# Optimization experiments

Hardware: AMD Instinct MI355X
Metric: run time of the kernel (lower is better)

The kernel has to match this reference:

```python
import jax, jax.numpy as jnp
import numpy as np

B, P, D = 16, 512, 1024   # batch, num wordpieces, bert_dim (roberta-large)
W, T, E = 400, 32, 64     # num words, num triggers (spans), num entities (spans)
H = 600                   # hidden_num of role_idn_ffn


def _make_idxs(rng, b, m, n, max_len):
    # [start, end) intervals with 0 <= start < end <= n, sorted starts per row
    starts = np.sort(rng.integers(0, n - 1, size=(b, m)), axis=1)
    ends = np.minimum(starts + rng.integers(1, max_len + 1, size=(b, m)), n)
    ends = np.maximum(ends, starts + 1)
    return np.stack([starts, ends], axis=-1).astype(np.int32)


def setup_inputs() -> dict:
    key = jax.random.key(0)
    k1, k2, k3 = jax.random.split(key, 3)
    rng = np.random.default_rng(0)
    return {
        "piece_reprs": jax.random.normal(k1, (B, P, D), dtype=jnp.float32),
        "word_idxs": jnp.asarray(_make_idxs(rng, B, W, P, 4)),
        "trigger_idxs": jnp.asarray(_make_idxs(rng, B, T, W, 8)),
        "entity_idxs": jnp.asarray(_make_idxs(rng, B, E, W, 12)),
        "W0": jax.random.normal(k2, (4 * D, H), dtype=jnp.float32) * 0.02,
        "b0": jnp.zeros((H,), dtype=jnp.float32),
        "W1": jax.random.normal(k3, (H, 2), dtype=jnp.float32) * 0.02,
        "b1": jnp.zeros((2,), dtype=jnp.float32),
    }


def _segment_mean(x, idxs):
    """Mean of x[b, start:end] per interval. x: [B,N,Dm], idxs: [B,M,2] -> [B,M,Dm].
    Vectorized replacement of the nested-loop slice+mean via inclusive prefix sums."""
    cs = jnp.concatenate([jnp.zeros_like(x[:, :1]), jnp.cumsum(x, axis=1)], axis=1)  # [B,N+1,Dm]
    s = jnp.take_along_axis(cs, idxs[:, :, 0:1], axis=1)  # [B,M,Dm]
    e = jnp.take_along_axis(cs, idxs[:, :, 1:2], axis=1)  # [B,M,Dm]
    lens = (idxs[:, :, 1] - idxs[:, :, 0]).astype(x.dtype)[:, :, None]
    return (e - s) / lens


def reference(piece_reprs, word_idxs, trigger_idxs, entity_idxs, W0, b0, W1, b1):
    # encode(): wordpiece -> word averaging (compute_word_reps_avg)
    word_reprs = _segment_mean(piece_reprs, word_idxs)          # [B, W, D]
    # scores(): span mean pooling (compute_span_reprs)
    trig = _segment_mean(word_reprs, trigger_idxs)              # [B, T, D]
    ent = _segment_mean(word_reprs, entity_idxs)                # [B, E, D]
    b, t, d = trig.shape
    e = ent.shape[1]
    # compute_binary_reprs: all (trigger, entity) pairs, trigger index varies slowly
    t_rep = jnp.broadcast_to(trig[:, :, None, :], (b, t, e, d)).reshape(b, t * e, d)
    e_rep = jnp.broadcast_to(ent[:, None, :, :], (b, t, e, d)).reshape(b, t * e, d)
    role = jnp.concatenate([t_rep, e_rep, t_rep * e_rep, jnp.abs(t_rep - e_rep)], axis=-1)  # [B,T*E,4D]
    # role_idn_ffn: Linears([4D, H, 2]) with relu between layers (dropout=0 at eval)
    h = jax.nn.relu(role @ W0 + b0)
    return h @ W1 + b1                                          # [B, T*E, 2]
```

## Files before the change

### kernel.cpp

```cpp
#include <hip/hip_runtime.h>
#include <cstddef>
#include <cstdint>

typedef float f32x4 __attribute__((ext_vector_type(4)));
typedef __bf16 bf16x8 __attribute__((ext_vector_type(8)));

constexpr int NB = 16;
constexpr int NP = 512;
constexpr int ND = 1024;
constexpr int NW = 400;
constexpr int NT = 32;
constexpr int NE = 64;
constexpr int NH = 600;
constexpr int IMGP = 128 * 64;
constexpr int IMGQ = 320 * 32;

__device__ inline bf16x8 pack8(float a0, float a1, float a2, float a3,
                               float a4, float a5, float a6, float a7) {
    bf16x8 v;
    v[0] = (__bf16)a0; v[1] = (__bf16)a1; v[2] = (__bf16)a2; v[3] = (__bf16)a3;
    v[4] = (__bf16)a4; v[5] = (__bf16)a5; v[6] = (__bf16)a6; v[7] = (__bf16)a7;
    return v;
}

__device__ inline void dma16(const void* g, void* l) {
    __builtin_amdgcn_global_load_lds(
        (const __attribute__((address_space(1))) uint32_t*)g,
        (__attribute__((address_space(3))) uint32_t*)l, 16, 0, 0);
}

#define LGKM_BARRIER() \
    asm volatile("s_waitcnt lgkmcnt(0)\n\ts_barrier" ::: "memory")

template <int MAXW>
__device__ inline float4 span_mean_cols(const float* __restrict__ pbase,
                                        const int* __restrict__ wrow,
                                        int s, int e) {
    int nw = e - s;
    int ps[MAXW], pe[MAXW];
#pragma unroll
    for (int w = 0; w < MAXW; ++w) {
        bool act = w < nw;
        int ww = s + w;
        ps[w] = act ? wrow[2 * ww] : 0;
        pe[w] = act ? wrow[2 * ww + 1] : 0;
    }
    float4 acc = make_float4(0.f, 0.f, 0.f, 0.f);
#pragma unroll
    for (int cb = 0; cb < MAXW; cb += 4) {
#pragma unroll
        for (int w = cb; w < cb + 4; ++w) {
            float4 wa = make_float4(0.f, 0.f, 0.f, 0.f);
#pragma unroll
            for (int p = 0; p < 4; ++p) {
                if (ps[w] + p < pe[w]) {
                    float4 v =
                        *(const float4*)(pbase + (size_t)(ps[w] + p) * ND);
                    wa.x += v.x; wa.y += v.y; wa.z += v.z; wa.w += v.w;
                }
            }
            if (pe[w] > ps[w]) {
                float wi = 1.0f / (float)(pe[w] - ps[w]);
                acc.x += wa.x * wi; acc.y += wa.y * wi;
                acc.z += wa.z * wi; acc.w += wa.w * wi;
            }
        }
    }
    return acc;
}

__global__ __launch_bounds__(256) void prep_kernel(
    const float* __restrict__ piece, const int* __restrict__ widx,
    const int* __restrict__ tidx, const int* __restrict__ eidx,
    const float* __restrict__ W0, __bf16* __restrict__ W0pre,
    __bf16* __restrict__ W0pair, float* __restrict__ trig,
    float* __restrict__ ent, float* __restrict__ out, int out_size) {
    __shared__ float T[32][132];
    int id = blockIdx.x;
    int t = threadIdx.x;
    if (id < NB * (NT + NE)) {
        const int* idx;
        float* outp;
        int b;
        bool is_trig = id < NB * NT;
        if (is_trig) {
            b = id / NT; idx = tidx + id * 2; outp = trig + (size_t)id * ND;
        } else {
            int id2 = id - NB * NT;
            b = id2 / NE; idx = eidx + id2 * 2; outp = ent + (size_t)id2 * ND;
        }
        int s = idx[0], e = idx[1];
        int col = t * 4;
        const int* wrow = widx + b * NW * 2;
        const float* pbase = piece + (size_t)b * NP * ND + col;
        float4 acc = is_trig ? span_mean_cols<8>(pbase, wrow, s, e)
                             : span_mean_cols<12>(pbase, wrow, s, e);
        float inv = 1.0f / (float)(e - s);
        acc.x *= inv; acc.y *= inv; acc.z *= inv; acc.w *= inv;
        *(float4*)(outp + col) = acc;
    } else {
        int bid = id - NB * (NT + NE);
        if (bid < 160) {
            int kb = bid & 31, nc = bid >> 5;
            __bf16* img = W0pre + ((size_t)nc * 32 + kb) * IMGP;
#pragma unroll
            for (int h = 0; h < 2; ++h) {
                {
                    int kl = t >> 3;
                    int n0 = (t & 7) * 16;
                    int kg = kb * 64 + h * 32 + kl;
                    const float* src = W0 + (size_t)kg * NH + nc * 128 + n0;
#pragma unroll
                    for (int g = 0; g < 4; ++g) {
                        int n = nc * 128 + n0 + g * 4;
                        float4 v = (n < NH) ? *(const float4*)(src + g * 4)
                                            : make_float4(0.f, 0.f, 0.f, 0.f);
                        *(float4*)&T[kl][n0 + g * 4] = v;
                    }
                }
                __syncthreads();
#pragma unroll
                for (int s = 0; s < 2; ++s) {
                    int idx = s * 256 + t;
                    int row = idx >> 2, cl = idx & 3, c = h * 4 + cl;
                    bf16x8 v = pack8(T[cl * 8 + 0][row], T[cl * 8 + 1][row],
                                     T[cl * 8 + 2][row], T[cl * 8 + 3][row],
                                     T[cl * 8 + 4][row], T[cl * 8 + 5][row],
                                     T[cl * 8 + 6][row], T[cl * 8 + 7][row]);
                    *(bf16x8*)&img[row * 64 + ((c ^ (row & 7)) << 3)] = v;
                }
                __syncthreads();
            }
        } else if (bid < 672) {
            int e = bid - 160;
            int it = e & 63, nc = (e >> 6) & 1, zz = e >> 7;
            float (*Tp)[84] = reinterpret_cast<float(*)[84]>(&T[0][0]);
            {
                int kidx = t >> 3, part = t & 7;
                int korig = (kidx < 16) ? (2048 + it * 16 + kidx)
                                        : (3072 + it * 16 + (kidx - 16));
                const float* src = W0 + (size_t)korig * NH;
#pragma unroll
                for (int g = 0; g < 10; ++g) {
                    int n = nc * 320 + zz * 80 + part * 10 + g;
                    Tp[kidx][part * 10 + g] = (n < NH) ? src[n] : 0.0f;
                }
            }
            __syncthreads();
            __bf16* img = W0pair + ((size_t)nc * 64 + it) * IMGQ;
#pragma unroll
            for (int s = 0; s < 2; ++s) {
                int idx = s * 256 + t;
                if (idx < 320) {
                    int rloc = idx >> 2, c = idx & 3;
                    bf16x8 v = pack8(Tp[c * 8 + 0][rloc], Tp[c * 8 + 1][rloc],
                                     Tp[c * 8 + 2][rloc], Tp[c * 8 + 3][rloc],
                                     Tp[c * 8 + 4][rloc], Tp[c * 8 + 5][rloc],
                                     Tp[c * 8 + 6][rloc], Tp[c * 8 + 7][rloc]);
                    int rg = zz * 80 + rloc;
                    int slot = ((rg >> 1) + c) & 3;
                    *(bf16x8*)&img[rg * 32 + slot * 8] = v;
                }
            }
        } else {
            int j = ((bid - 672) * 256 + t) * 8;
            float4 z = make_float4(0.f, 0.f, 0.f, 0.f);
            if (j + 8 <= out_size) {
                *(float4*)(out + j) = z;
                *(float4*)(out + j + 4) = z;
            }
        }
    }
}

__global__ __launch_bounds__(256) void pre_mfma_kernel(
    const float* __restrict__ trig, const float* __restrict__ ent,
    const __bf16* __restrict__ W0pre, float* __restrict__ pre_t,
    float* __restrict__ pre_e) {
    __shared__ __bf16 As[2][64 * 64];
    __shared__ __bf16 Bs[3][64 * 64];
    int mt8 = blockIdx.x, ntile = blockIdx.y;
    const float* A;
    float* C;
    int kbofs, mbase;
    if (mt8 < 8) { A = trig; C = pre_t; kbofs = 0;  mbase = mt8 * 64; }
    else         { A = ent;  C = pre_e; kbofs = 16; mbase = (mt8 - 8) * 64; }
    int tid = threadIdx.x;
    int lane = tid & 63, w = tid >> 6, rw = w & 1, cw = w >> 1;
    int q = lane >> 4, l15 = lane & 15, sa = l15 & 7;
    int nc = ntile >> 1, half = ntile & 1;
    const __bf16* imgbase =
        W0pre + ((size_t)nc * 32 + kbofs) * IMGP + half * 4096;
    int ar = tid >> 2, seg = tid & 3;
    f32x4 acc[2][2] = {};
    float4 av[4];

    auto dma_bb = [&](int it, int buf) {
        const __bf16* img = imgbase + (size_t)it * IMGP;
#pragma unroll
        for (int i = 0; i < 2; ++i) {
            int idx = i * 4 + w;
            dma16(img + idx * 512 + lane * 8, (__bf16*)Bs[buf] + idx * 512);
        }
    };
    auto load_a = [&](int it) {
        const float* src = A + (size_t)(mbase + ar) * ND + it * 64;
#pragma unroll
        for (int i = 0; i < 2; ++i) {
            int c = seg * 2 + i;
            av[i * 2]     = *(const float4*)(src + c * 8);
            av[i * 2 + 1] = *(const float4*)(src + c * 8 + 4);
        }
    };
    auto write_a = [&](int buf) {
#pragma unroll
        for (int i = 0; i < 2; ++i) {
            int c = seg * 2 + i;
            float4 a0 = av[i * 2], a1 = av[i * 2 + 1];
            *(bf16x8*)&As[buf][ar * 64 + ((c ^ (ar & 7)) << 3)] =
                pack8(a0.x, a0.y, a0.z, a0.w, a1.x, a1.y, a1.z, a1.w);
        }
    };
    auto mfma_t = [&](int abuf, int bbuf) {
#pragma unroll
        for (int ks = 0; ks < 2; ++ks) {
            int coff = ((q ^ sa) ^ (ks << 2)) << 3;
            bf16x8 af[2];
#pragma unroll
            for (int mt = 0; mt < 2; ++mt)
                af[mt] = *(const bf16x8*)&As[abuf][(32 * rw + 16 * mt + l15) * 64 + coff];
#pragma unroll
            for (int nt = 0; nt < 2; ++nt) {
                bf16x8 bf = *(const bf16x8*)&Bs[bbuf][(32 * cw + 16 * nt + l15) * 64 + coff];
#pragma unroll
                for (int mt = 0; mt < 2; ++mt)
                    acc[mt][nt] = __builtin_amdgcn_mfma_f32_16x16x32_bf16(
                        af[mt], bf, acc[mt][nt], 0, 0, 0);
            }
        }
    };

    load_a(0);
    dma_bb(0, 0);
    dma_bb(1, 1);
    write_a(0);
    __syncthreads();

    int bc = 0, bp = 2;
    for (int it = 0; it < 16; ++it) {
        int acur = it & 1, anxt = acur ^ 1;
        if (it < 15) load_a(it + 1);
        if (it < 14) dma_bb(it + 2, bp);
        __builtin_amdgcn_s_setprio(1);
        mfma_t(acur, bc);
        __builtin_amdgcn_s_setprio(0);
        if (it < 15) write_a(anxt);
        LGKM_BARRIER();
        bc = (bc == 2) ? 0 : bc + 1;
        bp = (bp == 2) ? 0 : bp + 1;
    }

#pragma unroll
    for (int mt = 0; mt < 2; ++mt)
#pragma unroll
        for (int r = 0; r < 4; ++r) {
            float* crow =
                C + (size_t)(mbase + 32 * rw + 16 * mt + 4 * q + r) * NH;
#pragma unroll
            for (int nt = 0; nt < 2; ++nt) {
                int n = ntile * 64 + 32 * cw + 16 * nt + l15;
                if (n < NH) crow[n] = acc[mt][nt][r];
            }
        }
}

__global__ __launch_bounds__(256, 2) void pair_mfma_kernel(
    const float* __restrict__ trig, const float* __restrict__ ent,
    const __bf16* __restrict__ W0pair, const float* __restrict__ b0,
    const float* __restrict__ pre_t, const float* __restrict__ pre_e,
    const float* __restrict__ W1, const float* __restrict__ b1,
    float* __restrict__ out) {
    __shared__ __bf16 Xs[2][128 * 32];
    __shared__ __bf16 Bs[2][320 * 32];
    __shared__ float Ts[2048];
    int b = blockIdx.x, tp = blockIdx.y, nc = blockIdx.z;
    int tid = threadIdx.x;
    int lane = tid & 63, w = tid >> 6, rw = w & 1, cw = w >> 1;
    int q = lane >> 4, l15 = lane & 15;
    int xr = tid >> 1, xh = tid & 1;
    const float* t0row = trig + (size_t)(b * NT + tp * 2) * ND;
    const float* erow = ent + (size_t)(b * NE + (xr & 63)) * ND;
    const __bf16* imgbase = W0pair + (size_t)nc * 64 * IMGQ;
    f32x4 acc[4][10] = {};
    float4 efA0, efA1, efB0, efB1;

    auto dma_b = [&](int it, int buf) {
        const __bf16* img = imgbase + (size_t)it * IMGQ + w * 2560;
        __bf16* lds = &Bs[buf][w * 2560];
#pragma unroll
        for (int i = 0; i < 5; ++i)
            dma16(img + i * 512 + lane * 8, lds + i * 512);
    };
    auto load_eA = [&](int it) {
        const float* er = erow + it * 16 + xh * 8;
        efA0 = *(const float4*)er;
        efA1 = *(const float4*)(er + 4);
    };
    auto load_eB = [&](int it) {
        const float* er = erow + it * 16 + xh * 8;
        efB0 = *(const float4*)er;
        efB1 = *(const float4*)(er + 4);
    };
    auto write_x = [&](int it, int buf, float4 e0, float4 e1) {
        const float* tsp = &Ts[(xr >> 6) * 1024 + it * 16 + xh * 8];
        float4 t0 = *(const float4*)tsp;
        float4 t1 = *(const float4*)(tsp + 4);
        float tf[8], ef[8];
        tf[0] = t0.x; tf[1] = t0.y; tf[2] = t0.z; tf[3] = t0.w;
        tf[4] = t1.x; tf[5] = t1.y; tf[6] = t1.z; tf[7] = t1.w;
        ef[0] = e0.x; ef[1] = e0.y; ef[2] = e0.z; ef[3] = e0.w;
        ef[4] = e1.x; ef[5] = e1.y; ef[6] = e1.z; ef[7] = e1.w;
        int sp = (((xr >> 1) + xh) & 3) * 8;
        int sd = (((xr >> 1) + 2 + xh) & 3) * 8;
        __bf16* xb = &Xs[buf][xr * 32];
        *(bf16x8*)(xb + sp) = pack8(
            tf[0] * ef[0], tf[1] * ef[1], tf[2] * ef[2], tf[3] * ef[3],
            tf[4] * ef[4], tf[5] * ef[5], tf[6] * ef[6], tf[7] * ef[7]);
        *(bf16x8*)(xb + sd) = pack8(
            fabsf(tf[0] - ef[0]), fabsf(tf[1] - ef[1]),
            fabsf(tf[2] - ef[2]), fabsf(tf[3] - ef[3]),
            fabsf(tf[4] - ef[4]), fabsf(tf[5] - ef[5]),
            fabsf(tf[6] - ef[6]), fabsf(tf[7] - ef[7]));
    };
    auto mfma_tile = [&](int buf) {
        const __bf16* X = Xs[buf];
        const __bf16* Bb = Bs[buf];
        bf16x8 af[4];
#pragma unroll
        for (int mt = 0; mt < 4; ++mt) {
            int r = 64 * rw + 16 * mt + l15;
            af[mt] = *(const bf16x8*)&X[r * 32 + (((r >> 1) + q) & 3) * 8];
        }
        __builtin_amdgcn_s_setprio(1);
#pragma unroll
        for (int nt = 0; nt < 10; ++nt) {
            int r = 160 * cw + 16 * nt + l15;
            bf16x8 bv = *(const bf16x8*)&Bb[r * 32 + (((r >> 1) + q) & 3) * 8];
#pragma unroll
            for (int mt = 0; mt < 4; ++mt)
                acc[mt][nt] = __builtin_amdgcn_mfma_f32_16x16x32_bf16(
                    af[mt], bv, acc[mt][nt], 0, 0, 0);
        }
        __builtin_amdgcn_s_setprio(0);
    };

    {
        int k0 = (tid & 127) * 8;
        int row = tid >> 7;
        const float* src = t0row + row * ND + k0;
        float4 va = *(const float4*)src;
        float4 vb = *(const float4*)(src + 4);
        *(float4*)&Ts[row * 1024 + k0] = va;
        *(float4*)&Ts[row * 1024 + k0 + 4] = vb;
    }
    load_eA(0);
    dma_b(0, 0);
    __syncthreads();
    load_eB(1);
    write_x(0, 0, efA0, efA1);
    __syncthreads();

    for (int itp = 0; itp < 32; ++itp) {
        int it0 = itp * 2;
        int it1 = it0 + 1;
        if (it0 < 62) load_eA(it0 + 2);
        dma_b(it0 + 1, 1);
        write_x(it0 + 1, 1, efB0, efB1);
        mfma_tile(0);
        __syncthreads();
        if (it1 < 62) load_eB(it1 + 2);
        if (it1 < 63) {
            dma_b(it1 + 1, 0);
            write_x(it1 + 1, 0, efA0, efA1);
        }
        mfma_tile(1);
        __syncthreads();
    }

    int tglob = b * NT + tp * 2 + rw;
    const float* preT = pre_t + (size_t)tglob * NH;
    float w10[10], w11[10], b0v[10], ptv[10];
    int nbase = nc * 320 + 160 * cw + l15;
#pragma unroll
    for (int nt = 0; nt < 10; ++nt) {
        int n = nbase + 16 * nt;
        bool v = n < NH;
        w10[nt] = v ? W1[2 * n] : 0.f;
        w11[nt] = v ? W1[2 * n + 1] : 0.f;
        b0v[nt] = v ? b0[n] : 0.f;
        ptv[nt] = v ? preT[n] : 0.f;
    }
    float b10 = b1[0], b11 = b1[1];
    bool lead = (l15 == 0);
    bool addb = (nc == 0) && (cw == 0);
#pragma unroll
    for (int mt = 0; mt < 4; ++mt) {
#pragma unroll
        for (int r = 0; r < 4; ++r) {
            int e = 16 * mt + 4 * q + r;
            const float* preE = pre_e + (size_t)(b * NE + e) * NH;
            float s0 = 0.f, s1 = 0.f;
#pragma unroll
            for (int nt = 0; nt < 10; ++nt) {
                int n = nbase + 16 * nt;
                float pe = (n < NH) ? preE[n] : 0.f;
                float h = acc[mt][nt][r] + ptv[nt] + pe + b0v[nt];
                h = fmaxf(h, 0.f);
                s0 += h * w10[nt];
                s1 += h * w11[nt];
            }
#pragma unroll
            for (int m = 8; m >= 1; m >>= 1) {
                s0 += __shfl_xor(s0, m);
                s1 += __shfl_xor(s1, m);
            }
            if (lead) {
                if (addb) { s0 += b10; s1 += b11; }
                float* o = out + ((size_t)(tglob * NE + e)) * 2;
                atomicAdd(o, s0);
                atomicAdd(o + 1, s1);
            }
        }
    }
}

extern "C" void kernel_launch(void* const* d_in, const int* in_sizes, int n_in,
                              void* d_out, int out_size, void* d_ws,
                              size_t ws_size, hipStream_t stream) {
    const float* piece = (const float*)d_in[0];
    const int* widx = (const int*)d_in[1];
    const int* tidx = (const int*)d_in[2];
    const int* eidx = (const int*)d_in[3];
    const float* W0 = (const float*)d_in[4];
    const float* b0 = (const float*)d_in[5];
    const float* W1 = (const float*)d_in[6];
    const float* b1 = (const float*)d_in[7];
    float* out = (float*)d_out;

    float* ws = (float*)d_ws;
    float* trig = ws;
    float* ent = trig + (size_t)NB * NT * ND;
    float* pre_t = ent + (size_t)NB * NE * ND;
    float* pre_e = pre_t + (size_t)NB * NT * NH;
    __bf16* W0pre = (__bf16*)(pre_e + (size_t)NB * NE * NH);
    __bf16* W0pair = W0pre + (size_t)5 * 32 * IMGP;

    int nprep = NB * (NT + NE) + 704;
    prep_kernel<<<nprep, 256, 0, stream>>>(piece, widx, tidx, eidx, W0, W0pre,
                                           W0pair, trig, ent, out, out_size);
    pre_mfma_kernel<<<dim3(24, 10), 256, 0, stream>>>(trig, ent, W0pre,
                                                      pre_t, pre_e);
    pair_mfma_kernel<<<dim3(16, 16, 2), 256, 0, stream>>>(
        trig, ent, W0pair, b0, pre_t, pre_e, W1, b1, out);
}
```

Before: 203.9 us.

## Split pair MFMA blocks to one trigger each for higher occupancy

Each pair_mfma block now handles a single trigger (64 pair rows) instead of two, doubling the grid to 16x32x2. The per-wave accumulator tile shrinks from 4x10 to 4x5 MFMA tiles and LDS usage drops, so launch bounds rise to 3 blocks per CU. The cost is that the W0pair B tiles are streamed twice as often, since each block reuses them across half as many rows, and there are more atomics per output element.

```diff
diff --git a/kernel.cpp b/kernel.cpp
--- a/kernel.cpp
+++ b/kernel.cpp
@@ -274,24 +274,25 @@
         }
 }
 
-__global__ __launch_bounds__(256, 2) void pair_mfma_kernel(
+__global__ __launch_bounds__(256, 3) void pair_mfma_kernel(
     const float* __restrict__ trig, const float* __restrict__ ent,
     const __bf16* __restrict__ W0pair, const float* __restrict__ b0,
     const float* __restrict__ pre_t, const float* __restrict__ pre_e,
     const float* __restrict__ W1, const float* __restrict__ b1,
     float* __restrict__ out) {
-    __shared__ __bf16 Xs[2][128 * 32];
+    __shared__ __bf16 Xs[2][64 * 32];
     __shared__ __bf16 Bs[2][320 * 32];
-    __shared__ float Ts[2048];
+    __shared__ float Ts[1024];
     int b = blockIdx.x, tp = blockIdx.y, nc = blockIdx.z;
     int tid = threadIdx.x;
-    int lane = tid & 63, w = tid >> 6, rw = w & 1, cw = w >> 1;
+    int lane = tid & 63, w = tid >> 6;
+    int cw = w;
     int q = lane >> 4, l15 = lane & 15;
-    int xr = tid >> 1, xh = tid & 1;
-    const float* t0row = trig + (size_t)(b * NT + tp * 2) * ND;
-    const float* erow = ent + (size_t)(b * NE + (xr & 63)) * ND;
+    int xr = tid >> 2, xq = tid & 3;
+    const float* t0row = trig + (size_t)(b * NT + tp) * ND;
+    const float* erow = ent + (size_t)(b * NE + xr) * ND;
     const __bf16* imgbase = W0pair + (size_t)nc * 64 * IMGQ;
-    f32x4 acc[4][10] = {};
+    f32x4 acc[4][5] = {};
     float4 efA0, efA1, efB0, efB1;
 
     auto dma_b = [&](int it, int buf) {
@@ -302,17 +303,17 @@
             dma16(img + i * 512 + lane * 8, lds + i * 512);
     };
     auto load_eA = [&](int it) {
-        const float* er = erow + it * 16 + xh * 8;
+        const float* er = erow + it * 16 + (xq & 1) * 8;
         efA0 = *(const float4*)er;
         efA1 = *(const float4*)(er + 4);
     };
     auto load_eB = [&](int it) {
-        const float* er = erow + it * 16 + xh * 8;
+        const float* er = erow + it * 16 + (xq & 1) * 8;
         efB0 = *(const float4*)er;
         efB1 = *(const float4*)(er + 4);
     };
     auto write_x = [&](int it, int buf, float4 e0, float4 e1) {
-        const float* tsp = &Ts[(xr >> 6) * 1024 + it * 16 + xh * 8];
+        const float* tsp = &Ts[it * 16 + (xq & 1) * 8];
         float4 t0 = *(const float4*)tsp;
         float4 t1 = *(const float4*)(tsp + 4);
         float tf[8], ef[8];
@@ -320,17 +321,17 @@
         tf[4] = t1.x; tf[5] = t1.y; tf[6] = t1.z; tf[7] = t1.w;
         ef[0] = e0.x; ef[1] = e0.y; ef[2] = e0.z; ef[3] = e0.w;
         ef[4] = e1.x; ef[5] = e1.y; ef[6] = e1.z; ef[7] = e1.w;
-        int sp = (((xr >> 1) + xh) & 3) * 8;
-        int sd = (((xr >> 1) + 2 + xh) & 3) * 8;
-        __bf16* xb = &Xs[buf][xr * 32];
-        *(bf16x8*)(xb + sp) = pack8(
-            tf[0] * ef[0], tf[1] * ef[1], tf[2] * ef[2], tf[3] * ef[3],
-            tf[4] * ef[4], tf[5] * ef[5], tf[6] * ef[6], tf[7] * ef[7]);
-        *(bf16x8*)(xb + sd) = pack8(
-            fabsf(tf[0] - ef[0]), fabsf(tf[1] - ef[1]),
-            fabsf(tf[2] - ef[2]), fabsf(tf[3] - ef[3]),
-            fabsf(tf[4] - ef[4]), fabsf(tf[5] - ef[5]),
-            fabsf(tf[6] - ef[6]), fabsf(tf[7] - ef[7]));
+        bool prod = (xq < 2);
+        float vj[8];
+#pragma unroll
+        for (int j = 0; j < 8; ++j) {
+            float p = tf[j] * ef[j];
+            float d = fabsf(tf[j] - ef[j]);
+            vj[j] = prod ? p : d;
+        }
+        int slot = ((xr >> 1) + xq) & 3;
+        *(bf16x8*)&Xs[buf][xr * 32 + slot * 8] =
+            pack8(vj[0], vj[1], vj[2], vj[3], vj[4], vj[5], vj[6], vj[7]);
     };
     auto mfma_tile = [&](int buf) {
         const __bf16* X = Xs[buf];
@@ -338,13 +339,13 @@
         bf16x8 af[4];
 #pragma unroll
         for (int mt = 0; mt < 4; ++mt) {
-            int r = 64 * rw + 16 * mt + l15;
+            int r = 16 * mt + l15;
             af[mt] = *(const bf16x8*)&X[r * 32 + (((r >> 1) + q) & 3) * 8];
         }
         __builtin_amdgcn_s_setprio(1);
 #pragma unroll
-        for (int nt = 0; nt < 10; ++nt) {
-            int r = 160 * cw + 16 * nt + l15;
+        for (int nt = 0; nt < 5; ++nt) {
+            int r = 80 * cw + 16 * nt + l15;
             bf16x8 bv = *(const bf16x8*)&Bb[r * 32 + (((r >> 1) + q) & 3) * 8];
 #pragma unroll
             for (int mt = 0; mt < 4; ++mt)
@@ -354,15 +355,7 @@
         __builtin_amdgcn_s_setprio(0);
     };
 
-    {
-        int k0 = (tid & 127) * 8;
-        int row = tid >> 7;
-        const float* src = t0row + row * ND + k0;
-        float4 va = *(const float4*)src;
-        float4 vb = *(const float4*)(src + 4);
-        *(float4*)&Ts[row * 1024 + k0] = va;
-        *(float4*)&Ts[row * 1024 + k0 + 4] = vb;
-    }
+    *(float4*)&Ts[tid * 4] = *(const float4*)(t0row + tid * 4);
     load_eA(0);
     dma_b(0, 0);
     __syncthreads();
@@ -387,12 +380,12 @@
         __syncthreads();
     }
 
-    int tglob = b * NT + tp * 2 + rw;
+    int tglob = b * NT + tp;
     const float* preT = pre_t + (size_t)tglob * NH;
-    float w10[10], w11[10], b0v[10], ptv[10];
-    int nbase = nc * 320 + 160 * cw + l15;
-#pragma unroll
-    for (int nt = 0; nt < 10; ++nt) {
+    float w10[5], w11[5], b0v[5], ptv[5];
+    int nbase = nc * 320 + 80 * cw + l15;
+#pragma unroll
+    for (int nt = 0; nt < 5; ++nt) {
         int n = nbase + 16 * nt;
         bool v = n < NH;
         w10[nt] = v ? W1[2 * n] : 0.f;
@@ -411,7 +404,7 @@
             const float* preE = pre_e + (size_t)(b * NE + e) * NH;
             float s0 = 0.f, s1 = 0.f;
 #pragma unroll
-            for (int nt = 0; nt < 10; ++nt) {
+            for (int nt = 0; nt < 5; ++nt) {
                 int n = nbase + 16 * nt;
                 float pe = (n < NH) ? preE[n] : 0.f;
                 float h = acc[mt][nt][r] + ptv[nt] + pe + b0v[nt];
@@ -460,6 +453,6 @@
                                            W0pair, trig, ent, out, out_size);
     pre_mfma_kernel<<<dim3(24, 10), 256, 0, stream>>>(trig, ent, W0pre,
                                                       pre_t, pre_e);
-    pair_mfma_kernel<<<dim3(16, 16, 2), 256, 0, stream>>>(
+    pair_mfma_kernel<<<dim3(16, 32, 2), 256, 0, stream>>>(
         trig, ent, W0pair, b0, pre_t, pre_e, W1, b1, out);
 }
```

New measurement: 245.2 us. +20.3%, slower.

## Build MFMA A-fragments in registers instead of staging pair features in LDS

Applied to the files above, without the earlier changes.

The product and abs-difference pair features are now computed straight into each lane's MFMA A operand: every lane loads its own entity rows from global memory and the trigger slice from LDS. This removes the Xs shared buffer, its writes and reads, and one barrier per k-step, and simplifies the loop to one iteration per k-step. In exchange each lane issues more global loads (four entity rows per step, redundant across waves), holds more registers, and computes both product and difference only to select one. Entity loads are now prefetched just one step ahead, so less latency is hidden.

```diff
diff --git a/kernel.cpp b/kernel.cpp
--- a/kernel.cpp
+++ b/kernel.cpp
@@ -280,19 +280,22 @@
     const float* __restrict__ pre_t, const float* __restrict__ pre_e,
     const float* __restrict__ W1, const float* __restrict__ b1,
     float* __restrict__ out) {
-    __shared__ __bf16 Xs[2][128 * 32];
     __shared__ __bf16 Bs[2][320 * 32];
     __shared__ float Ts[2048];
     int b = blockIdx.x, tp = blockIdx.y, nc = blockIdx.z;
     int tid = threadIdx.x;
     int lane = tid & 63, w = tid >> 6, rw = w & 1, cw = w >> 1;
     int q = lane >> 4, l15 = lane & 15;
-    int xr = tid >> 1, xh = tid & 1;
+    int kh = q & 1;
+    bool prod = (q < 2);
     const float* t0row = trig + (size_t)(b * NT + tp * 2) * ND;
-    const float* erow = ent + (size_t)(b * NE + (xr & 63)) * ND;
     const __bf16* imgbase = W0pair + (size_t)nc * 64 * IMGQ;
+    const float* ep0 = ent + (size_t)(b * NE + 0 + l15) * ND + kh * 8;
+    const float* ep1 = ep0 + 16 * ND;
+    const float* ep2 = ep0 + 32 * ND;
+    const float* ep3 = ep0 + 48 * ND;
     f32x4 acc[4][10] = {};
-    float4 efA0, efA1, efB0, efB1;
+    float4 ea0, ea1, eb0, eb1, ec0, ec1, ed0, ed1;
 
     auto dma_b = [&](int it, int buf) {
         const __bf16* img = imgbase + (size_t)it * IMGQ + w * 2560;
@@ -301,57 +304,28 @@
         for (int i = 0; i < 5; ++i)
             dma16(img + i * 512 + lane * 8, lds + i * 512);
     };
-    auto load_eA = [&](int it) {
-        const float* er = erow + it * 16 + xh * 8;
-        efA0 = *(const float4*)er;
-        efA1 = *(const float4*)(er + 4);
-    };
-    auto load_eB = [&](int it) {
-        const float* er = erow + it * 16 + xh * 8;
-        efB0 = *(const float4*)er;
-        efB1 = *(const float4*)(er + 4);
-    };
-    auto write_x = [&](int it, int buf, float4 e0, float4 e1) {
-        const float* tsp = &Ts[(xr >> 6) * 1024 + it * 16 + xh * 8];
-        float4 t0 = *(const float4*)tsp;
-        float4 t1 = *(const float4*)(tsp + 4);
-        float tf[8], ef[8];
-        tf[0] = t0.x; tf[1] = t0.y; tf[2] = t0.z; tf[3] = t0.w;
-        tf[4] = t1.x; tf[5] = t1.y; tf[6] = t1.z; tf[7] = t1.w;
-        ef[0] = e0.x; ef[1] = e0.y; ef[2] = e0.z; ef[3] = e0.w;
-        ef[4] = e1.x; ef[5] = e1.y; ef[6] = e1.z; ef[7] = e1.w;
-        int sp = (((xr >> 1) + xh) & 3) * 8;
-        int sd = (((xr >> 1) + 2 + xh) & 3) * 8;
-        __bf16* xb = &Xs[buf][xr * 32];
-        *(bf16x8*)(xb + sp) = pack8(
-            tf[0] * ef[0], tf[1] * ef[1], tf[2] * ef[2], tf[3] * ef[3],
-            tf[4] * ef[4], tf[5] * ef[5], tf[6] * ef[6], tf[7] * ef[7]);
-        *(bf16x8*)(xb + sd) = pack8(
-            fabsf(tf[0] - ef[0]), fabsf(tf[1] - ef[1]),
-            fabsf(tf[2] - ef[2]), fabsf(tf[3] - ef[3]),
-            fabsf(tf[4] - ef[4]), fabsf(tf[5] - ef[5]),
-            fabsf(tf[6] - ef[6]), fabsf(tf[7] - ef[7]));
-    };
-    auto mfma_tile = [&](int buf) {
-        const __bf16* X = Xs[buf];
-        const __bf16* Bb = Bs[buf];
-        bf16x8 af[4];
-#pragma unroll
-        for (int mt = 0; mt < 4; ++mt) {
-            int r = 64 * rw + 16 * mt + l15;
-            af[mt] = *(const bf16x8*)&X[r * 32 + (((r >> 1) + q) & 3) * 8];
-        }
-        __builtin_amdgcn_s_setprio(1);
-#pragma unroll
-        for (int nt = 0; nt < 10; ++nt) {
-            int r = 160 * cw + 16 * nt + l15;
-            bf16x8 bv = *(const bf16x8*)&Bb[r * 32 + (((r >> 1) + q) & 3) * 8];
-#pragma unroll
-            for (int mt = 0; mt < 4; ++mt)
-                acc[mt][nt] = __builtin_amdgcn_mfma_f32_16x16x32_bf16(
-                    af[mt], bv, acc[mt][nt], 0, 0, 0);
-        }
-        __builtin_amdgcn_s_setprio(0);
+    auto load_e = [&](int it) {
+        const float* p0 = ep0 + it * 16;
+        ea0 = *(const float4*)p0;  ea1 = *(const float4*)(p0 + 4);
+        const float* p1 = ep1 + it * 16;
+        eb0 = *(const float4*)p1;  eb1 = *(const float4*)(p1 + 4);
+        const float* p2 = ep2 + it * 16;
+        ec0 = *(const float4*)p2;  ec1 = *(const float4*)(p2 + 4);
+        const float* p3 = ep3 + it * 16;
+        ed0 = *(const float4*)p3;  ed1 = *(const float4*)(p3 + 4);
+    };
+    auto mk_af = [&](const float* tf, float4 x0, float4 x1) -> bf16x8 {
+        float e[8];
+        e[0] = x0.x; e[1] = x0.y; e[2] = x0.z; e[3] = x0.w;
+        e[4] = x1.x; e[5] = x1.y; e[6] = x1.z; e[7] = x1.w;
+        float v[8];
+#pragma unroll
+        for (int j = 0; j < 8; ++j) {
+            float p = tf[j] * e[j];
+            float d = fabsf(tf[j] - e[j]);
+            v[j] = prod ? p : d;
+        }
+        return pack8(v[0], v[1], v[2], v[3], v[4], v[5], v[6], v[7]);
     };
 
     {
@@ -363,27 +337,42 @@
         *(float4*)&Ts[row * 1024 + k0] = va;
         *(float4*)&Ts[row * 1024 + k0 + 4] = vb;
     }
-    load_eA(0);
+    load_e(0);
     dma_b(0, 0);
     __syncthreads();
-    load_eB(1);
-    write_x(0, 0, efA0, efA1);
-    __syncthreads();
-
-    for (int itp = 0; itp < 32; ++itp) {
-        int it0 = itp * 2;
-        int it1 = it0 + 1;
-        if (it0 < 62) load_eA(it0 + 2);
-        dma_b(it0 + 1, 1);
-        write_x(it0 + 1, 1, efB0, efB1);
-        mfma_tile(0);
-        __syncthreads();
-        if (it1 < 62) load_eB(it1 + 2);
-        if (it1 < 63) {
-            dma_b(it1 + 1, 0);
-            write_x(it1 + 1, 0, efA0, efA1);
-        }
-        mfma_tile(1);
+
+    for (int it = 0; it < 64; ++it) {
+        int cur = it & 1;
+        if (it < 63) dma_b(it + 1, cur ^ 1);
+        bf16x8 af[4];
+        {
+            const float* tsp = &Ts[rw * 1024 + it * 16 + kh * 8];
+            float4 t0 = *(const float4*)tsp;
+            float4 t1 = *(const float4*)(tsp + 4);
+            float tf[8];
+            tf[0] = t0.x; tf[1] = t0.y; tf[2] = t0.z; tf[3] = t0.w;
+            tf[4] = t1.x; tf[5] = t1.y; tf[6] = t1.z; tf[7] = t1.w;
+            af[0] = mk_af(tf, ea0, ea1);
+            af[1] = mk_af(tf, eb0, eb1);
+            af[2] = mk_af(tf, ec0, ec1);
+            af[3] = mk_af(tf, ed0, ed1);
+        }
+        if (it < 63) load_e(it + 1);
+        {
+            const __bf16* Bb = Bs[cur];
+            __builtin_amdgcn_s_setprio(1);
+#pragma unroll
+            for (int nt = 0; nt < 10; ++nt) {
+                int r = 160 * cw + 16 * nt + l15;
+                bf16x8 bv =
+                    *(const bf16x8*)&Bb[r * 32 + (((r >> 1) + q) & 3) * 8];
+#pragma unroll
+                for (int mt = 0; mt < 4; ++mt)
+                    acc[mt][nt] = __builtin_amdgcn_mfma_f32_16x16x32_bf16(
+                        af[mt], bv, acc[mt][nt], 0, 0, 0);
+            }
+            __builtin_amdgcn_s_setprio(0);
+        }
         __syncthreads();
     }
 
```

Measured after the change: 264.7 us. 29.9% more time.
